# Performance work log

Measured on AMD Instinct MI355X. Metric: run time of the kernel, lower is better.

The kernel has to match this reference:

```python
import jax, jax.numpy as jnp
import numpy as np

N = 20000      # nodes
E = 320000     # edges (avg degree 16)
D = 128        # emb_dim
L = 5          # num_layer
NV = 119       # node vocab (atom types)
EV = 5         # edge vocab (bond types)
BN_EPS = 1e-5


def setup_inputs() -> dict:
    key = jax.random.key(0)
    ks = jax.random.split(key, 8)
    s = 0.1
    return {
        "x": jax.random.randint(ks[0], (N,), 0, NV),
        "edge_index": jax.random.randint(ks[1], (2, E), 0, N),
        "edge_attr": jax.random.randint(ks[2], (E,), 0, EV),
        "node_emb1": jax.random.normal(ks[3], (NV, D), jnp.float32) * s,
        "node_emb2": jax.random.normal(ks[4], (NV, D), jnp.float32) * s,
        "edge_emb": jax.random.normal(ks[5], (2, L, EV, D), jnp.float32) * s,
        "eps": jnp.zeros((2, L), jnp.float32),
        "W": jax.random.normal(ks[6], (2, L, D, D), jnp.float32) / np.sqrt(D).astype(np.float32),
        "b": jnp.zeros((2, L, D), jnp.float32),
        "bn_gamma": jnp.ones((2, L, D), jnp.float32),
        "bn_beta": jnp.zeros((2, L, D), jnp.float32),
        "cross_unit": jnp.full((L, 2, 2), 0.5, jnp.float32),
    }


def gin_conv(h, src, dst, eattr, edge_tab, eps, W, b):
    # message: relu(x_j + edge_embedding), aggregated by add at target nodes
    msg = jax.nn.relu(h[src] + edge_tab[eattr])            # [E, D]
    agg = jax.ops.segment_sum(msg, dst, num_segments=h.shape[0])  # [N, D]
    return ((1.0 + eps) * h + agg) @ W.T + b               # mlp = single Linear


def batch_norm(h, gamma, beta):
    # training-mode BatchNorm1d over the node dimension (biased variance)
    mu = h.mean(axis=0)
    var = h.var(axis=0)
    return (h - mu) * jax.lax.rsqrt(var + BN_EPS) * gamma + beta


def reference(x, edge_index, edge_attr, node_emb1, node_emb2, edge_emb, eps, W, b,
              bn_gamma, bn_beta, cross_unit):
    src, dst = edge_index[0], edge_index[1]
    h1 = node_emb1[x]   # NodeEncoder tower 1
    h2 = node_emb2[x]   # NodeEncoder tower 2
    for l in range(L):
        a1 = gin_conv(h1, src, dst, edge_attr, edge_emb[0, l], eps[0, l], W[0, l], b[0, l])
        a1 = batch_norm(a1, bn_gamma[0, l], bn_beta[0, l])
        a2 = gin_conv(h2, src, dst, edge_attr, edge_emb[1, l], eps[1, l], W[1, l], b[1, l])
        a2 = batch_norm(a2, bn_gamma[1, l], bn_beta[1, l])
        if l < L - 1:
            a1 = jax.nn.relu(a1)
            a2 = jax.nn.relu(a2)
        # dropout: identity (eval mode / deterministic reference)
        # cross-stitch; note h_2 uses the UPDATED h_1 (faithful to source)
        c = cross_unit[l]
        n1 = c[0, 0] * a1 + c[0, 1] * a2
        n2 = c[1, 0] * n1 + c[1, 1] * a2
        h1, h2 = n1, n2
    return (h1, h2)  # JK == 'last'
```

## Files before the change

### kernel.cpp

```cpp
#include <hip/hip_runtime.h>

#define NN 20000
#define EE 320000
#define DD 128
#define LL 5
#define EVV 5
#define BNEPS 1e-5f
#define NB 313
#define EMB_BLOCKS 2500
#define CVT_BLOCKS 160
#define CNT_BLOCKS 1250

typedef __attribute__((ext_vector_type(8))) short bf8_t;
typedef __attribute__((ext_vector_type(4))) float f4_t;

__device__ inline unsigned short f2bf(float f) {
    union { float f; unsigned u; } v;
    v.f = f;
    unsigned r = v.u + 0x7fffu + ((v.u >> 16) & 1u);
    return (unsigned short)(r >> 16);
}
__device__ inline float bf2f(unsigned short h) {
    union { unsigned u; float f; } v;
    v.u = ((unsigned)h) << 16;
    return v.f;
}
__device__ inline float4 bf2f4(ushort4 u) {
    float4 f;
    f.x = bf2f(u.x); f.y = bf2f(u.y); f.z = bf2f(u.z); f.w = bf2f(u.w);
    return f;
}
__device__ inline float4 add4(float4 a, float4 b) {
    float4 r;
    r.x = a.x + b.x; r.y = a.y + b.y; r.z = a.z + b.z; r.w = a.w + b.w;
    return r;
}

__device__ inline void xform4(float4 v1, float4 v2,
                              float4 s1, float4 t1, float4 s2, float4 t2,
                              float c00, float c01, float c10, float c11,
                              int dorelu, float4& n1, float4& n2) {
    float x1, x2, m1, m2;
#define XE(f)                                                    \
    x1 = v1.f * s1.f + t1.f;                                     \
    x2 = v2.f * s2.f + t2.f;                                     \
    x1 = dorelu ? fmaxf(x1, 0.f) : x1;                           \
    x2 = dorelu ? fmaxf(x2, 0.f) : x2;                           \
    m1 = c00 * x1 + c01 * x2;                                    \
    m2 = c10 * m1 + c11 * x2;                                    \
    n1.f = m1;                                                   \
    n2.f = m2;
    XE(x) XE(y) XE(z) XE(w)
#undef XE
}

__device__ inline void acc_relu4(float4& a, float4 v, float4 e) {
    a.x += fmaxf(v.x + e.x, 0.f);
    a.y += fmaxf(v.y + e.y, 0.f);
    a.z += fmaxf(v.z + e.z, 0.f);
    a.w += fmaxf(v.w + e.w, 0.f);
}

__device__ inline void bn_coeffs(const float* __restrict__ statsL,
                                 const float* __restrict__ gall,
                                 const float* __restrict__ btall,
                                 int pl, int c,
                                 float4& s1, float4& t1, float4& s2, float4& t2) {
    const float inv = 1.0f / (float)NN;
    int ch = c * 4;
#define BNC(tw, sv, tv)                                                       \
    {                                                                         \
        const float* gp = gall + (size_t)((tw) * LL + pl) * DD + ch;          \
        const float* bp = btall + (size_t)((tw) * LL + pl) * DD + ch;         \
        float r[4];                                                           \
        _Pragma("unroll") for (int j = 0; j < 4; j++) {                       \
            float sum = statsL[(tw) * 256 + ch + j];                          \
            float sq = statsL[(tw) * 256 + 128 + ch + j];                     \
            float mu = sum * inv;                                             \
            float var = sq * inv - mu * mu;                                   \
            float rs = rsqrtf(var + BNEPS);                                   \
            float sc = rs * gp[j];                                            \
            r[j] = sc;                                                        \
            ((float*)&tv)[j] = bp[j] - mu * sc;                               \
        }                                                                     \
        sv.x = r[0]; sv.y = r[1]; sv.z = r[2]; sv.w = r[3];                   \
    }
    BNC(0, s1, t1)
    BNC(1, s2, t2)
#undef BNC
}


__global__ __launch_bounds__(256) void prep_kernel(
    const int* __restrict__ x,
    const float4* __restrict__ e1, const float4* __restrict__ e2,
    ushort4* __restrict__ yh, ushort4* __restrict__ yl,
    const float4* __restrict__ Wall,
    ushort4* __restrict__ Wbh, ushort4* __restrict__ Wbl,
    const int* __restrict__ dst, int* __restrict__ deg,
    float* __restrict__ stats) {
    int bid = blockIdx.x;
    int tid = threadIdx.x;
    if (bid < EMB_BLOCKS) {
        int idx = bid * 256 + tid;
        int r = idx >> 5, c = idx & 31;
        int v = x[r];
        float4 w1 = e1[v * 32 + c];
        float4 w2 = e2[v * 32 + c];
        ushort4 h, l;
        h.x = f2bf(w1.x); h.y = f2bf(w1.y); h.z = f2bf(w1.z); h.w = f2bf(w1.w);
        l.x = f2bf(w1.x - bf2f(h.x)); l.y = f2bf(w1.y - bf2f(h.y));
        l.z = f2bf(w1.z - bf2f(h.z)); l.w = f2bf(w1.w - bf2f(h.w));
        yh[(size_t)r * 64 + c] = h;
        yl[(size_t)r * 64 + c] = l;
        h.x = f2bf(w2.x); h.y = f2bf(w2.y); h.z = f2bf(w2.z); h.w = f2bf(w2.w);
        l.x = f2bf(w2.x - bf2f(h.x)); l.y = f2bf(w2.y - bf2f(h.y));
        l.z = f2bf(w2.z - bf2f(h.z)); l.w = f2bf(w2.w - bf2f(h.w));
        yh[(size_t)r * 64 + 32 + c] = h;
        yl[(size_t)r * 64 + 32 + c] = l;
    } else if (bid < EMB_BLOCKS + CVT_BLOCKS) {
        int i = (bid - EMB_BLOCKS) * 256 + tid;
        float4 w = Wall[i];
        ushort4 oh, ol;
        oh.x = f2bf(w.x); oh.y = f2bf(w.y); oh.z = f2bf(w.z); oh.w = f2bf(w.w);
        ol.x = f2bf(w.x - bf2f(oh.x));
        ol.y = f2bf(w.y - bf2f(oh.y));
        ol.z = f2bf(w.z - bf2f(oh.z));
        ol.w = f2bf(w.w - bf2f(oh.w));
        Wbh[i] = oh;
        Wbl[i] = ol;
    } else if (bid < EMB_BLOCKS + CVT_BLOCKS + CNT_BLOCKS) {
        int e = (bid - EMB_BLOCKS - CVT_BLOCKS) * 256 + tid;
        atomicAdd(&deg[dst[e]], 1);
    } else {
#pragma unroll
        for (int i = 0; i < 10; i++) stats[i * 256 + tid] = 0.f;
    }
}


__global__ __launch_bounds__(1024) void scan_kernel(const int* __restrict__ deg,
                                                    int* __restrict__ offs,
                                                    int* __restrict__ pos) {
    __shared__ int wsum[16];
    int t = threadIdx.x;
    int lane = t & 63, wv = t >> 6;
    int base = t * 20;
    int loc[20];
    int s = 0;
#pragma unroll
    for (int i = 0; i < 20; i++) {
        int j = base + i;
        int d = (j < NN) ? deg[j] : 0;
        loc[i] = d;
        s += d;
    }
    int incl = s;
#pragma unroll
    for (int o = 1; o < 64; o <<= 1) {
        int v = __shfl_up(incl, o, 64);
        if (lane >= o) incl += v;
    }
    if (lane == 63) wsum[wv] = incl;
    __syncthreads();
    if (t < 16) {
        int v = wsum[t];
        int iv = v;
#pragma unroll
        for (int o = 1; o < 16; o <<= 1) {
            int u = __shfl_up(iv, o, 64);
            if (t >= o) iv += u;
        }
        wsum[t] = iv - v;
    }
    __syncthreads();
    int run = wsum[wv] + (incl - s);
#pragma unroll
    for (int i = 0; i < 20; i++) {
        int j = base + i;
        if (j < NN) {
            offs[j] = run;
            pos[j] = run;
            run += loc[i];
        }
    }
}

__global__ __launch_bounds__(256) void scatter_kernel(const int* __restrict__ src,
                                                      const int* __restrict__ dst,
                                                      const int* __restrict__ eattr,
                                                      int* __restrict__ pos,
                                                      int2* __restrict__ erec) {
    int e = blockIdx.x * 256 + threadIdx.x;
    if (e < EE) {
        int d = dst[e];
        int p = atomicAdd(&pos[d], 1);
        erec[p] = make_int2(src[e], eattr[e]);
    }
}


__global__ __launch_bounds__(256) void aggregate_kernel(
    const ushort4* __restrict__ yh, const ushort4* __restrict__ yl,
    const float* __restrict__ etab, int layer,
    const int* __restrict__ offs, const int* __restrict__ deg,
    const int2* __restrict__ erec, const float* __restrict__ epsall,
    const float* __restrict__ statsPrev,
    const float* __restrict__ gall, const float* __restrict__ btall,
    const float* __restrict__ crossp, int dobn,
    unsigned short* __restrict__ ubuf) {
    int tid = threadIdx.x;
    int node = blockIdx.x * 4 + (tid >> 6);
    int lane = tid & 63;
    int half = lane >> 5;
    int c = lane & 31;
    const float4* t1v = (const float4*)(etab + (size_t)(0 * LL + layer) * EVV * DD);
    const float4* t2v = (const float4*)(etab + (size_t)(1 * LL + layer) * EVV * DD);

    float4 s1, t1, s2, t2;
    float c00, c01, c10, c11;
    if (dobn) {
        bn_coeffs(statsPrev, gall, btall, layer - 1, c, s1, t1, s2, t2);
        c00 = crossp[0]; c01 = crossp[1]; c10 = crossp[2]; c11 = crossp[3];
    } else {
        s1.x = s1.y = s1.z = s1.w = 1.f;
        s2 = s1;
        t1.x = t1.y = t1.z = t1.w = 0.f;
        t2 = t1;
        c00 = 1.f; c01 = 0.f; c10 = 0.f; c11 = 1.f;
    }
    int dorelu = dobn;

    int off = offs[node];
    int dg = deg[node];
    float4 a1; a1.x = a1.y = a1.z = a1.w = 0.f;
    float4 a2; a2.x = a2.y = a2.z = a2.w = 0.f;
    int i = 0;
    for (; i + 8 <= dg; i += 8) {
        int2 r0 = erec[off + i + half];
        int2 r1 = erec[off + i + 2 + half];
        int2 r2 = erec[off + i + 4 + half];
        int2 r3 = erec[off + i + 6 + half];
        ushort4 u10 = yh[(size_t)r0.x * 64 + c];
        ushort4 u20 = yh[(size_t)r0.x * 64 + 32 + c];
        ushort4 u11 = yh[(size_t)r1.x * 64 + c];
        ushort4 u21 = yh[(size_t)r1.x * 64 + 32 + c];
        ushort4 u12 = yh[(size_t)r2.x * 64 + c];
        ushort4 u22 = yh[(size_t)r2.x * 64 + 32 + c];
        ushort4 u13 = yh[(size_t)r3.x * 64 + c];
        ushort4 u23 = yh[(size_t)r3.x * 64 + 32 + c];
        float4 e10 = t1v[r0.y * 32 + c];
        float4 e20 = t2v[r0.y * 32 + c];
        float4 e11 = t1v[r1.y * 32 + c];
        float4 e21 = t2v[r1.y * 32 + c];
        float4 e12 = t1v[r2.y * 32 + c];
        float4 e22 = t2v[r2.y * 32 + c];
        float4 e13 = t1v[r3.y * 32 + c];
        float4 e23 = t2v[r3.y * 32 + c];
        float4 n1, n2;
        xform4(bf2f4(u10), bf2f4(u20), s1, t1, s2, t2, c00, c01, c10, c11, dorelu, n1, n2);
        acc_relu4(a1, n1, e10);
        acc_relu4(a2, n2, e20);
        xform4(bf2f4(u11), bf2f4(u21), s1, t1, s2, t2, c00, c01, c10, c11, dorelu, n1, n2);
        acc_relu4(a1, n1, e11);
        acc_relu4(a2, n2, e21);
        xform4(bf2f4(u12), bf2f4(u22), s1, t1, s2, t2, c00, c01, c10, c11, dorelu, n1, n2);
        acc_relu4(a1, n1, e12);
        acc_relu4(a2, n2, e22);
        xform4(bf2f4(u13), bf2f4(u23), s1, t1, s2, t2, c00, c01, c10, c11, dorelu, n1, n2);
        acc_relu4(a1, n1, e13);
        acc_relu4(a2, n2, e23);
    }
    for (; i < dg; i += 2) {
        int j = i + half;
        bool valid = (j < dg);
        int e = off + (valid ? j : 0);
        int2 r = erec[e];
        ushort4 v1u = yh[(size_t)r.x * 64 + c];
        ushort4 v2u = yh[(size_t)r.x * 64 + 32 + c];
        float4 e1 = t1v[r.y * 32 + c];
        float4 e2 = t2v[r.y * 32 + c];
        float4 n1, n2;
        xform4(bf2f4(v1u), bf2f4(v2u), s1, t1, s2, t2, c00, c01, c10, c11, dorelu, n1, n2);
        if (valid) {
            acc_relu4(a1, n1, e1);
            acc_relu4(a2, n2, e2);
        }
    }
    a1.x += __shfl_xor(a1.x, 32, 64);
    a1.y += __shfl_xor(a1.y, 32, 64);
    a1.z += __shfl_xor(a1.z, 32, 64);
    a1.w += __shfl_xor(a1.w, 32, 64);
    a2.x += __shfl_xor(a2.x, 32, 64);
    a2.y += __shfl_xor(a2.y, 32, 64);
    a2.z += __shfl_xor(a2.z, 32, 64);
    a2.w += __shfl_xor(a2.w, 32, 64);

    float4 vs1 = add4(bf2f4(yh[(size_t)node * 64 + c]), bf2f4(yl[(size_t)node * 64 + c]));
    float4 vs2 = add4(bf2f4(yh[(size_t)node * 64 + 32 + c]), bf2f4(yl[(size_t)node * 64 + 32 + c]));
    float4 hn1, hn2;
    xform4(vs1, vs2, s1, t1, s2, t2, c00, c01, c10, c11, dorelu, hn1, hn2);
    float ep = 1.0f + epsall[half * LL + layer];
    float4 hs = half ? hn2 : hn1;
    float4 aa = half ? a2 : a1;
    float4 u;
    u.x = ep * hs.x + aa.x;
    u.y = ep * hs.y + aa.y;
    u.z = ep * hs.z + aa.z;
    u.w = ep * hs.w + aa.w;
    ushort4 uh, ul;
    uh.x = f2bf(u.x); uh.y = f2bf(u.y); uh.z = f2bf(u.z); uh.w = f2bf(u.w);
    ul.x = f2bf(u.x - bf2f(uh.x));
    ul.y = f2bf(u.y - bf2f(uh.y));
    ul.z = f2bf(u.z - bf2f(uh.z));
    ul.w = f2bf(u.w - bf2f(uh.w));
    ushort4* uo = (ushort4*)ubuf;
    uo[(size_t)node * 128 + half * 32 + c] = uh;
    uo[(size_t)node * 128 + 64 + half * 32 + c] = ul;
}


__global__ __launch_bounds__(256) void gemm_mfma_kernel(
    const unsigned short* __restrict__ ubuf,
    const unsigned short* __restrict__ Wbh, const unsigned short* __restrict__ Wbl,
    const float* __restrict__ ball, int layer,
    unsigned short* __restrict__ yh, unsigned short* __restrict__ yl,
    float* __restrict__ statsL) {
    __shared__ float sP[2][4][DD];
    int tid = threadIdx.x;
    int tower = blockIdx.y;
    const bf8_t* Wh8 = (const bf8_t*)(Wbh + (size_t)(tower * LL + layer) * DD * DD);
    const bf8_t* Wl8 = (const bf8_t*)(Wbl + (size_t)(tower * LL + layer) * DD * DD);
    const float* bias = ball + (size_t)(tower * LL + layer) * DD;
    const bf8_t* u8 = (const bf8_t*)ubuf;

    int wave = tid >> 6, lane = tid & 63;
    int quad = lane >> 4, m = lane & 15;
    int row_base = blockIdx.x * 64 + wave * 16;

    f4_t acc[8];
#pragma unroll
    for (int nt = 0; nt < 8; nt++) {
        acc[nt][0] = 0.f; acc[nt][1] = 0.f; acc[nt][2] = 0.f; acc[nt][3] = 0.f;
    }

    int aidx = (row_base + m) * 64 + tower * 16;
#pragma unroll
    for (int kt = 0; kt < 4; kt++) {
        bf8_t ah = u8[aidx + kt * 4 + quad];
        bf8_t al = u8[aidx + 32 + kt * 4 + quad];
#pragma unroll
        for (int nt = 0; nt < 8; nt++) {
            bf8_t bh = Wh8[(nt * 16 + m) * 16 + kt * 4 + quad];
            bf8_t bl = Wl8[(nt * 16 + m) * 16 + kt * 4 + quad];
            acc[nt] = __builtin_amdgcn_mfma_f32_16x16x32_bf16(ah, bh, acc[nt], 0, 0, 0);
            acc[nt] = __builtin_amdgcn_mfma_f32_16x16x32_bf16(al, bh, acc[nt], 0, 0, 0);
            acc[nt] = __builtin_amdgcn_mfma_f32_16x16x32_bf16(ah, bl, acc[nt], 0, 0, 0);
        }
    }

#pragma unroll
    for (int nt = 0; nt < 8; nt++) {
        int col = nt * 16 + m;
        float bv = bias[col];
        float s = 0.f, q = 0.f;
#pragma unroll
        for (int r = 0; r < 4; r++) {
            int row = row_base + quad * 4 + r;
            if (row < NN) {
                float v = acc[nt][r] + bv;
                unsigned short hi = f2bf(v);
                size_t oidx = (size_t)row * 256 + tower * DD + col;
                yh[oidx] = hi;
                yl[oidx] = f2bf(v - bf2f(hi));
                s += v;
                q += v * v;
            }
        }
        s += __shfl_xor(s, 16, 64); s += __shfl_xor(s, 32, 64);
        q += __shfl_xor(q, 16, 64); q += __shfl_xor(q, 32, 64);
        if (quad == 0) {
            sP[0][wave][col] = s;
            sP[1][wave][col] = q;
        }
    }
    __syncthreads();
    int ch = tid & 127, sq = tid >> 7;
    float v = sP[sq][0][ch] + sP[sq][1][ch] + sP[sq][2][ch] + sP[sq][3][ch];
    atomicAdd(&statsL[tower * 256 + tid], v);
}


__global__ __launch_bounds__(256) void bn_final_kernel(
    const ushort4* __restrict__ yh, const ushort4* __restrict__ yl,
    float4* __restrict__ o1, float4* __restrict__ o2,
    const float* __restrict__ statsL,
    const float* __restrict__ gall, const float* __restrict__ btall,
    const float* __restrict__ crossp) {
    int idx = blockIdx.x * 256 + threadIdx.x;
    int r = idx >> 5, c = idx & 31;
    float4 s1, t1, s2, t2;
    bn_coeffs(statsL, gall, btall, LL - 1, c, s1, t1, s2, t2);
    float c00 = crossp[0], c01 = crossp[1], c10 = crossp[2], c11 = crossp[3];
    float4 v1 = add4(bf2f4(yh[(size_t)r * 64 + c]), bf2f4(yl[(size_t)r * 64 + c]));
    float4 v2 = add4(bf2f4(yh[(size_t)r * 64 + 32 + c]), bf2f4(yl[(size_t)r * 64 + 32 + c]));
    float4 n1, n2;
    xform4(v1, v2, s1, t1, s2, t2, c00, c01, c10, c11, 0, n1, n2);
    o1[(size_t)r * 32 + c] = n1;
    o2[(size_t)r * 32 + c] = n2;
}


extern "C" void kernel_launch(void* const* d_in, const int* in_sizes, int n_in,
                              void* d_out, int out_size, void* d_ws, size_t ws_size,
                              hipStream_t stream) {
    const int* x = (const int*)d_in[0];
    const int* eidx = (const int*)d_in[1];
    const int* eattr = (const int*)d_in[2];
    const float* emb1 = (const float*)d_in[3];
    const float* emb2 = (const float*)d_in[4];
    const float* etab = (const float*)d_in[5];
    const float* epsv = (const float*)d_in[6];
    const float* Wall = (const float*)d_in[7];
    const float* ball = (const float*)d_in[8];
    const float* gall = (const float*)d_in[9];
    const float* btall = (const float*)d_in[10];
    const float* cross = (const float*)d_in[11];
    float* out = (float*)d_out;

    const size_t ND = (size_t)NN * DD;
    char* p = (char*)d_ws;
    unsigned short* yh = (unsigned short*)p;   p += (size_t)NN * 256 * 2;
    unsigned short* yl = (unsigned short*)p;   p += (size_t)NN * 256 * 2;
    unsigned short* ubuf = (unsigned short*)p; p += (size_t)NN * 512 * 2;
    unsigned short* Wbh = (unsigned short*)p;  p += (size_t)2 * LL * DD * DD * 2;
    unsigned short* Wbl = (unsigned short*)p;  p += (size_t)2 * LL * DD * DD * 2;
    int* deg = (int*)p;               p += (size_t)NN * 4;
    int* offs = (int*)p;              p += (size_t)NN * 4;
    int* pos = (int*)p;               p += (size_t)NN * 4;
    int2* erec = (int2*)p;            p += (size_t)EE * 8;
    float* stats = (float*)p;         p += (size_t)LL * 512 * 4;

    const int* src = eidx;
    const int* dst = eidx + EE;

    hipMemsetAsync(deg, 0, (size_t)NN * 4, stream);
    prep_kernel<<<EMB_BLOCKS + CVT_BLOCKS + CNT_BLOCKS + 1, 256, 0, stream>>>(
        x, (const float4*)emb1, (const float4*)emb2,
        (ushort4*)yh, (ushort4*)yl,
        (const float4*)Wall, (ushort4*)Wbh, (ushort4*)Wbl, dst, deg, stats);
    scan_kernel<<<1, 1024, 0, stream>>>(deg, offs, pos);
    scatter_kernel<<<EE / 256, 256, 0, stream>>>(src, dst, eattr, pos, erec);

    for (int l = 0; l < LL; l++) {
        aggregate_kernel<<<NN / 4, 256, 0, stream>>>(
            (const ushort4*)yh, (const ushort4*)yl, etab, l, offs, deg, erec, epsv,
            stats + (size_t)(l > 0 ? l - 1 : 0) * 512, gall, btall,
            cross + (l > 0 ? (l - 1) * 4 : 0), (l > 0) ? 1 : 0, ubuf);
        dim3 g(NB, 2);
        gemm_mfma_kernel<<<g, 256, 0, stream>>>(ubuf, Wbh, Wbl, ball, l, yh, yl,
                                                stats + (size_t)l * 512);
    }
    bn_final_kernel<<<(NN * 32) / 256, 256, 0, stream>>>(
        (const ushort4*)yh, (const ushort4*)yl, (float4*)out, (float4*)(out + ND),
        stats + (size_t)(LL - 1) * 512, gall, btall, cross + (LL - 1) * 4);
}
```

Measured before the change: 579.4 us.

## Widen aggregate gathers to 16-byte vectors and stage GEMM epilogue through LDS

The aggregate kernel now gives each lane 8 channels and handles 4 edges per wave in parallel, loading 16-byte bf16 vectors instead of 8-byte ones. The edge embedding table is pre-converted to bf16 once in the prep kernel. The GEMM epilogue writes results into a padded shared-memory tile and then stores coalesced 16-byte hi/lo bf16 vectors, replacing scattered 2-byte stores. Edge embeddings are now rounded to bf16, which loses some precision and adds shared memory and register pressure.

```diff
diff --git a/kernel.cpp b/kernel.cpp
--- a/kernel.cpp
+++ b/kernel.cpp
@@ -13,6 +13,7 @@
 
 typedef __attribute__((ext_vector_type(8))) short bf8_t;
 typedef __attribute__((ext_vector_type(4))) float f4_t;
+typedef __attribute__((ext_vector_type(8))) unsigned short us8;
 
 __device__ inline unsigned short f2bf(float f) {
     union { float f; unsigned u; } v;
@@ -52,13 +53,6 @@
     n2.f = m2;
     XE(x) XE(y) XE(z) XE(w)
 #undef XE
-}
-
-__device__ inline void acc_relu4(float4& a, float4 v, float4 e) {
-    a.x += fmaxf(v.x + e.x, 0.f);
-    a.y += fmaxf(v.y + e.y, 0.f);
-    a.z += fmaxf(v.z + e.z, 0.f);
-    a.w += fmaxf(v.w + e.w, 0.f);
 }
 
 __device__ inline void bn_coeffs(const float* __restrict__ statsL,
@@ -98,7 +92,8 @@
     const float4* __restrict__ Wall,
     ushort4* __restrict__ Wbh, ushort4* __restrict__ Wbl,
     const int* __restrict__ dst, int* __restrict__ deg,
-    float* __restrict__ stats) {
+    float* __restrict__ stats,
+    const float* __restrict__ etab, unsigned short* __restrict__ etb_bf) {
     int bid = blockIdx.x;
     int tid = threadIdx.x;
     if (bid < EMB_BLOCKS) {
@@ -135,6 +130,7 @@
     } else {
 #pragma unroll
         for (int i = 0; i < 10; i++) stats[i * 256 + tid] = 0.f;
+        for (int i = tid; i < 2 * LL * EVV * DD; i += 256) etb_bf[i] = f2bf(etab[i]);
     }
 }
 
@@ -201,122 +197,142 @@
 
 
 __global__ __launch_bounds__(256) void aggregate_kernel(
-    const ushort4* __restrict__ yh, const ushort4* __restrict__ yl,
-    const float* __restrict__ etab, int layer,
+    const us8* __restrict__ yh8, const us8* __restrict__ yl8,
+    const unsigned short* __restrict__ etb, int layer,
     const int* __restrict__ offs, const int* __restrict__ deg,
     const int2* __restrict__ erec, const float* __restrict__ epsall,
     const float* __restrict__ statsPrev,
     const float* __restrict__ gall, const float* __restrict__ btall,
     const float* __restrict__ crossp, int dobn,
-    unsigned short* __restrict__ ubuf) {
+    us8* __restrict__ uo8) {
     int tid = threadIdx.x;
     int node = blockIdx.x * 4 + (tid >> 6);
     int lane = tid & 63;
-    int half = lane >> 5;
-    int c = lane & 31;
-    const float4* t1v = (const float4*)(etab + (size_t)(0 * LL + layer) * EVV * DD);
-    const float4* t2v = (const float4*)(etab + (size_t)(1 * LL + layer) * EVV * DD);
-
-    float4 s1, t1, s2, t2;
+    int slot = lane >> 4;
+    int c8 = lane & 15;
+    int ch0 = c8 * 8;
+    const us8* et0 = (const us8*)(etb + (size_t)(0 * LL + layer) * EVV * DD);
+    const us8* et1 = (const us8*)(etb + (size_t)(1 * LL + layer) * EVV * DD);
+
+    float s1[8], t1[8], s2[8], t2[8];
     float c00, c01, c10, c11;
+    int dorelu = dobn;
     if (dobn) {
-        bn_coeffs(statsPrev, gall, btall, layer - 1, c, s1, t1, s2, t2);
+        const float inv = 1.0f / (float)NN;
+        int pl = layer - 1;
+        const float* g0 = gall + (size_t)(0 * LL + pl) * DD + ch0;
+        const float* b0 = btall + (size_t)(0 * LL + pl) * DD + ch0;
+        const float* g1 = gall + (size_t)(1 * LL + pl) * DD + ch0;
+        const float* b1 = btall + (size_t)(1 * LL + pl) * DD + ch0;
+#pragma unroll
+        for (int j = 0; j < 8; j++) {
+            float sum = statsPrev[ch0 + j];
+            float sq = statsPrev[128 + ch0 + j];
+            float mu = sum * inv;
+            float var = sq * inv - mu * mu;
+            float sc = rsqrtf(var + BNEPS) * g0[j];
+            s1[j] = sc;
+            t1[j] = b0[j] - mu * sc;
+            float sum2 = statsPrev[256 + ch0 + j];
+            float sq2 = statsPrev[256 + 128 + ch0 + j];
+            float mu2 = sum2 * inv;
+            float var2 = sq2 * inv - mu2 * mu2;
+            float sc2 = rsqrtf(var2 + BNEPS) * g1[j];
+            s2[j] = sc2;
+            t2[j] = b1[j] - mu2 * sc2;
+        }
         c00 = crossp[0]; c01 = crossp[1]; c10 = crossp[2]; c11 = crossp[3];
     } else {
-        s1.x = s1.y = s1.z = s1.w = 1.f;
-        s2 = s1;
-        t1.x = t1.y = t1.z = t1.w = 0.f;
-        t2 = t1;
+#pragma unroll
+        for (int j = 0; j < 8; j++) { s1[j] = 1.f; t1[j] = 0.f; s2[j] = 1.f; t2[j] = 0.f; }
         c00 = 1.f; c01 = 0.f; c10 = 0.f; c11 = 1.f;
     }
-    int dorelu = dobn;
 
     int off = offs[node];
     int dg = deg[node];
-    float4 a1; a1.x = a1.y = a1.z = a1.w = 0.f;
-    float4 a2; a2.x = a2.y = a2.z = a2.w = 0.f;
+    float a1[8], a2[8];
+#pragma unroll
+    for (int k = 0; k < 8; k++) { a1[k] = 0.f; a2[k] = 0.f; }
+
+    auto process = [&](us8 h0, us8 h1, us8 e0, us8 e1, bool valid) {
+#pragma unroll
+        for (int k = 0; k < 8; k++) {
+            float x1 = bf2f(h0[k]) * s1[k] + t1[k];
+            float x2 = bf2f(h1[k]) * s2[k] + t2[k];
+            x1 = dorelu ? fmaxf(x1, 0.f) : x1;
+            x2 = dorelu ? fmaxf(x2, 0.f) : x2;
+            float m1 = c00 * x1 + c01 * x2;
+            float m2 = c10 * m1 + c11 * x2;
+            if (valid) {
+                a1[k] += fmaxf(m1 + bf2f(e0[k]), 0.f);
+                a2[k] += fmaxf(m2 + bf2f(e1[k]), 0.f);
+            }
+        }
+    };
+
     int i = 0;
     for (; i + 8 <= dg; i += 8) {
-        int2 r0 = erec[off + i + half];
-        int2 r1 = erec[off + i + 2 + half];
-        int2 r2 = erec[off + i + 4 + half];
-        int2 r3 = erec[off + i + 6 + half];
-        ushort4 u10 = yh[(size_t)r0.x * 64 + c];
-        ushort4 u20 = yh[(size_t)r0.x * 64 + 32 + c];
-        ushort4 u11 = yh[(size_t)r1.x * 64 + c];
-        ushort4 u21 = yh[(size_t)r1.x * 64 + 32 + c];
-        ushort4 u12 = yh[(size_t)r2.x * 64 + c];
-        ushort4 u22 = yh[(size_t)r2.x * 64 + 32 + c];
-        ushort4 u13 = yh[(size_t)r3.x * 64 + c];
-        ushort4 u23 = yh[(size_t)r3.x * 64 + 32 + c];
-        float4 e10 = t1v[r0.y * 32 + c];
-        float4 e20 = t2v[r0.y * 32 + c];
-        float4 e11 = t1v[r1.y * 32 + c];
-        float4 e21 = t2v[r1.y * 32 + c];
-        float4 e12 = t1v[r2.y * 32 + c];
-        float4 e22 = t2v[r2.y * 32 + c];
-        float4 e13 = t1v[r3.y * 32 + c];
-        float4 e23 = t2v[r3.y * 32 + c];
-        float4 n1, n2;
-        xform4(bf2f4(u10), bf2f4(u20), s1, t1, s2, t2, c00, c01, c10, c11, dorelu, n1, n2);
-        acc_relu4(a1, n1, e10);
-        acc_relu4(a2, n2, e20);
-        xform4(bf2f4(u11), bf2f4(u21), s1, t1, s2, t2, c00, c01, c10, c11, dorelu, n1, n2);
-        acc_relu4(a1, n1, e11);
-        acc_relu4(a2, n2, e21);
-        xform4(bf2f4(u12), bf2f4(u22), s1, t1, s2, t2, c00, c01, c10, c11, dorelu, n1, n2);
-        acc_relu4(a1, n1, e12);
-        acc_relu4(a2, n2, e22);
-        xform4(bf2f4(u13), bf2f4(u23), s1, t1, s2, t2, c00, c01, c10, c11, dorelu, n1, n2);
-        acc_relu4(a1, n1, e13);
-        acc_relu4(a2, n2, e23);
-    }
-    for (; i < dg; i += 2) {
-        int j = i + half;
-        bool valid = (j < dg);
+        int2 ra = erec[off + i + slot];
+        int2 rb = erec[off + i + 4 + slot];
+        us8 h0a = yh8[(size_t)ra.x * 32 + c8];
+        us8 h1a = yh8[(size_t)ra.x * 32 + 16 + c8];
+        us8 h0b = yh8[(size_t)rb.x * 32 + c8];
+        us8 h1b = yh8[(size_t)rb.x * 32 + 16 + c8];
+        us8 e0a = et0[ra.y * 16 + c8];
+        us8 e1a = et1[ra.y * 16 + c8];
+        us8 e0b = et0[rb.y * 16 + c8];
+        us8 e1b = et1[rb.y * 16 + c8];
+        process(h0a, h1a, e0a, e1a, true);
+        process(h0b, h1b, e0b, e1b, true);
+    }
+    for (; i < dg; i += 4) {
+        int j = i + slot;
+        bool valid = j < dg;
         int e = off + (valid ? j : 0);
         int2 r = erec[e];
-        ushort4 v1u = yh[(size_t)r.x * 64 + c];
-        ushort4 v2u = yh[(size_t)r.x * 64 + 32 + c];
-        float4 e1 = t1v[r.y * 32 + c];
-        float4 e2 = t2v[r.y * 32 + c];
-        float4 n1, n2;
-        xform4(bf2f4(v1u), bf2f4(v2u), s1, t1, s2, t2, c00, c01, c10, c11, dorelu, n1, n2);
-        if (valid) {
-            acc_relu4(a1, n1, e1);
-            acc_relu4(a2, n2, e2);
-        }
-    }
-    a1.x += __shfl_xor(a1.x, 32, 64);
-    a1.y += __shfl_xor(a1.y, 32, 64);
-    a1.z += __shfl_xor(a1.z, 32, 64);
-    a1.w += __shfl_xor(a1.w, 32, 64);
-    a2.x += __shfl_xor(a2.x, 32, 64);
-    a2.y += __shfl_xor(a2.y, 32, 64);
-    a2.z += __shfl_xor(a2.z, 32, 64);
-    a2.w += __shfl_xor(a2.w, 32, 64);
-
-    float4 vs1 = add4(bf2f4(yh[(size_t)node * 64 + c]), bf2f4(yl[(size_t)node * 64 + c]));
-    float4 vs2 = add4(bf2f4(yh[(size_t)node * 64 + 32 + c]), bf2f4(yl[(size_t)node * 64 + 32 + c]));
-    float4 hn1, hn2;
-    xform4(vs1, vs2, s1, t1, s2, t2, c00, c01, c10, c11, dorelu, hn1, hn2);
-    float ep = 1.0f + epsall[half * LL + layer];
-    float4 hs = half ? hn2 : hn1;
-    float4 aa = half ? a2 : a1;
-    float4 u;
-    u.x = ep * hs.x + aa.x;
-    u.y = ep * hs.y + aa.y;
-    u.z = ep * hs.z + aa.z;
-    u.w = ep * hs.w + aa.w;
-    ushort4 uh, ul;
-    uh.x = f2bf(u.x); uh.y = f2bf(u.y); uh.z = f2bf(u.z); uh.w = f2bf(u.w);
-    ul.x = f2bf(u.x - bf2f(uh.x));
-    ul.y = f2bf(u.y - bf2f(uh.y));
-    ul.z = f2bf(u.z - bf2f(uh.z));
-    ul.w = f2bf(u.w - bf2f(uh.w));
-    ushort4* uo = (ushort4*)ubuf;
-    uo[(size_t)node * 128 + half * 32 + c] = uh;
-    uo[(size_t)node * 128 + 64 + half * 32 + c] = ul;
+        us8 h0 = yh8[(size_t)r.x * 32 + c8];
+        us8 h1 = yh8[(size_t)r.x * 32 + 16 + c8];
+        us8 e0 = et0[r.y * 16 + c8];
+        us8 e1 = et1[r.y * 16 + c8];
+        process(h0, h1, e0, e1, valid);
+    }
+
+#pragma unroll
+    for (int k = 0; k < 8; k++) {
+        a1[k] += __shfl_xor(a1[k], 16, 64);
+        a1[k] += __shfl_xor(a1[k], 32, 64);
+        a2[k] += __shfl_xor(a2[k], 16, 64);
+        a2[k] += __shfl_xor(a2[k], 32, 64);
+    }
+
+    us8 sh0 = yh8[(size_t)node * 32 + c8];
+    us8 sl0 = yl8[(size_t)node * 32 + c8];
+    us8 sh1 = yh8[(size_t)node * 32 + 16 + c8];
+    us8 sl1 = yl8[(size_t)node * 32 + 16 + c8];
+    float ep1 = 1.0f + epsall[0 * LL + layer];
+    float ep2 = 1.0f + epsall[1 * LL + layer];
+    us8 uh1, ul1, uh2, ul2;
+#pragma unroll
+    for (int k = 0; k < 8; k++) {
+        float v1 = bf2f(sh0[k]) + bf2f(sl0[k]);
+        float v2 = bf2f(sh1[k]) + bf2f(sl1[k]);
+        float x1 = v1 * s1[k] + t1[k];
+        float x2 = v2 * s2[k] + t2[k];
+        x1 = dorelu ? fmaxf(x1, 0.f) : x1;
+        x2 = dorelu ? fmaxf(x2, 0.f) : x2;
+        float m1 = c00 * x1 + c01 * x2;
+        float m2 = c10 * m1 + c11 * x2;
+        float u1 = ep1 * m1 + a1[k];
+        float u2 = ep2 * m2 + a2[k];
+        unsigned short h1u = f2bf(u1);
+        uh1[k] = h1u;
+        ul1[k] = f2bf(u1 - bf2f(h1u));
+        unsigned short h2u = f2bf(u2);
+        uh2[k] = h2u;
+        ul2[k] = f2bf(u2 - bf2f(h2u));
+    }
+    us8 pick = (slot == 0) ? uh1 : (slot == 1) ? uh2 : (slot == 2) ? ul1 : ul2;
+    uo8[(size_t)node * 64 + slot * 16 + c8] = pick;
 }
 
 
@@ -326,6 +342,7 @@
     const float* __restrict__ ball, int layer,
     unsigned short* __restrict__ yh, unsigned short* __restrict__ yl,
     float* __restrict__ statsL) {
+    __shared__ float accS[64 * 4 * 33];
     __shared__ float sP[2][4][DD];
     int tid = threadIdx.x;
     int tower = blockIdx.y;
@@ -363,19 +380,15 @@
     for (int nt = 0; nt < 8; nt++) {
         int col = nt * 16 + m;
         float bv = bias[col];
+        int cg = col >> 5, kk = col & 31;
         float s = 0.f, q = 0.f;
 #pragma unroll
         for (int r = 0; r < 4; r++) {
-            int row = row_base + quad * 4 + r;
-            if (row < NN) {
-                float v = acc[nt][r] + bv;
-                unsigned short hi = f2bf(v);
-                size_t oidx = (size_t)row * 256 + tower * DD + col;
-                yh[oidx] = hi;
-                yl[oidx] = f2bf(v - bf2f(hi));
-                s += v;
-                q += v * v;
-            }
+            int lrow = wave * 16 + quad * 4 + r;
+            int row = blockIdx.x * 64 + lrow;
+            float v = acc[nt][r] + bv;
+            accS[(lrow * 4 + cg) * 33 + kk] = v;
+            if (row < NN) { s += v; q += v * v; }
         }
         s += __shfl_xor(s, 16, 64); s += __shfl_xor(s, 32, 64);
         q += __shfl_xor(q, 16, 64); q += __shfl_xor(q, 32, 64);
@@ -385,6 +398,31 @@
         }
     }
     __syncthreads();
+
+    {
+        int lrow = tid >> 2, cg = tid & 3;
+        int grow = blockIdx.x * 64 + lrow;
+        if (grow < NN) {
+            const float* srcp = &accS[(lrow * 4 + cg) * 33];
+            us8* yhp = (us8*)yh;
+            us8* ylp = (us8*)yl;
+            size_t base = (size_t)grow * 32 + tower * 16 + cg * 4;
+#pragma unroll
+            for (int j = 0; j < 4; j++) {
+                us8 hv, lv;
+#pragma unroll
+                for (int k = 0; k < 8; k++) {
+                    float v = srcp[j * 8 + k];
+                    unsigned short h = f2bf(v);
+                    hv[k] = h;
+                    lv[k] = f2bf(v - bf2f(h));
+                }
+                yhp[base + j] = hv;
+                ylp[base + j] = lv;
+            }
+        }
+    }
+
     int ch = tid & 127, sq = tid >> 7;
     float v = sP[sq][0][ch] + sP[sq][1][ch] + sP[sq][2][ch] + sP[sq][3][ch];
     atomicAdd(&statsL[tower * 256 + tid], v);
@@ -435,6 +473,7 @@
     unsigned short* ubuf = (unsigned short*)p; p += (size_t)NN * 512 * 2;
     unsigned short* Wbh = (unsigned short*)p;  p += (size_t)2 * LL * DD * DD * 2;
     unsigned short* Wbl = (unsigned short*)p;  p += (size_t)2 * LL * DD * DD * 2;
+    unsigned short* etb_bf = (unsigned short*)p; p += (size_t)2 * LL * EVV * DD * 2;
     int* deg = (int*)p;               p += (size_t)NN * 4;
     int* offs = (int*)p;              p += (size_t)NN * 4;
     int* pos = (int*)p;               p += (size_t)NN * 4;
@@ -448,15 +487,16 @@
     prep_kernel<<<EMB_BLOCKS + CVT_BLOCKS + CNT_BLOCKS + 1, 256, 0, stream>>>(
         x, (const float4*)emb1, (const float4*)emb2,
         (ushort4*)yh, (ushort4*)yl,
-        (const float4*)Wall, (ushort4*)Wbh, (ushort4*)Wbl, dst, deg, stats);
+        (const float4*)Wall, (ushort4*)Wbh, (ushort4*)Wbl, dst, deg, stats,
+        etab, etb_bf);
     scan_kernel<<<1, 1024, 0, stream>>>(deg, offs, pos);
     scatter_kernel<<<EE / 256, 256, 0, stream>>>(src, dst, eattr, pos, erec);
 
     for (int l = 0; l < LL; l++) {
         aggregate_kernel<<<NN / 4, 256, 0, stream>>>(
-            (const ushort4*)yh, (const ushort4*)yl, etab, l, offs, deg, erec, epsv,
+            (const us8*)yh, (const us8*)yl, etb_bf, l, offs, deg, erec, epsv,
             stats + (size_t)(l > 0 ? l - 1 : 0) * 512, gall, btall,
-            cross + (l > 0 ? (l - 1) * 4 : 0), (l > 0) ? 1 : 0, ubuf);
+            cross + (l > 0 ? (l - 1) * 4 : 0), (l > 0) ? 1 : 0, (us8*)ubuf);
         dim3 g(NB, 2);
         gemm_mfma_kernel<<<g, 256, 0, stream>>>(ubuf, Wbh, Wbl, ball, l, yh, yl,
                                                 stats + (size_t)l * 512);
```

New measurement: 598.7 us. +3.3%, slower.
